# Performance work log

Measured on AMD Instinct MI355X. Metric: run time of the kernel, lower is better.

The kernel has to match this reference:

```python
import jax, jax.numpy as jnp
import numpy as np

SR = 16000
N_WT = 10
WT_LEN = 512
FIR_TAPS = 31
NU_C = 0.1
N_REFLECT = (FIR_TAPS - 1) // 2
B, L = 16, 160000


def setup_inputs() -> dict:
    key = jax.random.key(0)
    k1, k2, k3, k4 = jax.random.split(key, 4)
    # F0 in a realistic [100, 400) Hz range
    pitch = jax.random.uniform(k1, (B, L, 1), jnp.float32) * 300.0 + 100.0
    envelope = jax.random.uniform(k2, (B, L, 1), jnp.float32)
    # attention weights are 'already softmaxed' over the wavetable axis
    attention = jax.nn.softmax(jax.random.normal(k3, (B, L, N_WT), jnp.float32), axis=-1)
    # learned wavetables, init N(0, 0.01) as in the torch module (n_pure_harmonics=0)
    wavetables = jax.random.normal(k4, (N_WT, WT_LEN), jnp.float32) * 0.01
    # fixed windowed-sinc low-pass FIR (Type I), same construction as __init__
    n = np.arange(-(FIR_TAPS - 1) // 2, 1 + (FIR_TAPS - 1) // 2, dtype=np.float32)
    h = 2.0 * NU_C * np.sinc(2.0 * NU_C * n) * np.hamming(FIR_TAPS)
    fir_h = jnp.asarray(h, jnp.float32)
    return {"pitch": pitch, "envelope": envelope, "attention": attention,
            "wavetables": wavetables, "fir_h": fir_h}


def reference(pitch, envelope, attention, wavetables, fir_h):
    # circular ('reflect' in the repo's naming) pad each wavetable: (W, 512+2*15)
    wt_pad = jnp.concatenate(
        [wavetables[:, -N_REFLECT:], wavetables, wavetables[:, :N_REFLECT]], axis=1)
    # torch conv1d is cross-correlation; jnp.correlate 'valid' matches -> (W, 512)
    wt = jax.vmap(lambda x: jnp.correlate(x, fir_h, mode='valid'))(wt_pad)

    L_wt = WT_LEN
    freqs = pitch[..., 0]                       # (B, L)
    increment = (L_wt / SR) * freqs             # phase increment per sample
    # NOTE: faithful to torch code: increment[0] is the FIRST BATCH ROW (L,)
    index = jnp.cumsum(increment, axis=1) - increment[0]
    index = jnp.remainder(index, L_wt)
    index = jnp.where(L_wt - index < 1e-5, 0.0, index)
    idx_lo_f = jnp.floor(index)
    alpha = index - idx_lo_f                    # (B, L)
    i_lo = idx_lo_f.astype(jnp.int32)
    i_hi = jnp.ceil(index).astype(jnp.int32) % L_wt

    # gather all wavetables at once: (W, B, L)
    lo = jnp.take(wt, i_lo, axis=1)
    hi = jnp.take(wt, i_hi, axis=1)
    wave = lo + alpha[None, :, :] * (hi - lo)   # linear interpolation
    wave = jnp.transpose(wave, (1, 2, 0))       # (B, L, W)

    out = jnp.sum(wave * attention, axis=2, keepdims=True) * envelope  # (B, L, 1)
    return out
```

## Files before the change

kernel.cpp:

```cpp
#include <hip/hip_runtime.h>

#define N_WT_     10
#define WT_LEN_   512
#define FIR_TAPS_ 31
#define N_REFL_   15
#define B_        16
#define L_        160000

constexpr int   TPB   = 256;
constexpr float INCF  = 0.032f;
constexpr int   NG0   = L_ / 16;
constexpr int   NG1   = NG0 / 16;
constexpr int   NG2   = 40;
constexpr int   NG3   = 3;
constexpr int   CPB   = 5;

__global__ void fir_kernel(const float* __restrict__ wavetables,
                           const float* __restrict__ fir_h,
                           float* __restrict__ wt_out) {
    __shared__ float s_pad[WT_LEN_ + 2 * N_REFL_];
    __shared__ float s_h[FIR_TAPS_];
    const int w = blockIdx.x;
    const int i = threadIdx.x;
    if (i < FIR_TAPS_) s_h[i] = fir_h[i];
    for (int j = i; j < WT_LEN_ + 2 * N_REFL_; j += blockDim.x) {
        int src = (j + WT_LEN_ - N_REFL_) % WT_LEN_;
        s_pad[j] = wavetables[w * WT_LEN_ + src];
    }
    __syncthreads();
    float acc = 0.0f;
#pragma unroll
    for (int t = 0; t < FIR_TAPS_; ++t)
        acc = fmaf(s_h[t], s_pad[i + t], acc);
    wt_out[w * WT_LEN_ + i] = acc;
}

__global__ __launch_bounds__(TPB) void ysum_kernel(
        const float* __restrict__ pitch, float* __restrict__ y) {
    __shared__ float s_x[4096];
    const int b = blockIdx.y, bx = blockIdx.x, t = threadIdx.x;
    const float* prow = pitch + (size_t)b * L_;
    const int x0 = bx * 4096;
    for (int i = t; i < 4096; i += TPB) {
        int l = x0 + i;
        s_x[i] = (l < L_) ? INCF * prow[l] : 0.0f;
    }
    __syncthreads();
    const int g = bx * 256 + t;
    if (g < NG0) {
        const float* p = s_x + (g * 16 - x0);
        float acc = 0.0f;
        for (int i = 0; i < 16; ++i) acc += p[i];
        y[b * NG0 + g] = acc;
    }
}

__global__ __launch_bounds__(TPB) void scan_kernel(
        const float* __restrict__ y, float* __restrict__ S1) {
    __shared__ float s_y[NG0];
    __shared__ float s_S1[NG0];
    __shared__ float s_z[NG1];
    __shared__ float s_S2[NG1];
    __shared__ float s_w[NG2], s_S3[NG2];
    __shared__ float s_v[NG3], s_S4[NG3];
    const int b = blockIdx.x, t = threadIdx.x;
    const float* yrow = y + (size_t)b * NG0;
    for (int i = t; i < NG0; i += TPB) s_y[i] = yrow[i];
    __syncthreads();
    for (int j = t; j < NG1; j += TPB) {
        float a = 0.0f;
        for (int i = 0; i < 16; ++i) a += s_y[16 * j + i];
        s_z[j] = a;
    }
    __syncthreads();
    if (t < NG2) {
        float a = 0.0f;
        int hi = min(16 * t + 16, NG1);
        for (int i = 16 * t; i < hi; ++i) a += s_z[i];
        s_w[t] = a;
    }
    __syncthreads();
    if (t < NG3) {
        float a = 0.0f;
        int hi = min(16 * t + 16, NG2);
        for (int i = 16 * t; i < hi; ++i) a += s_w[i];
        s_v[t] = a;
    }
    __syncthreads();
    if (t == 0) {
        float run = 0.0f;
        for (int m = 0; m < NG3; ++m) { run += s_v[m]; s_S4[m] = run; }
    }
    __syncthreads();
    if (t < NG2) {
        float a = 0.0f;
        for (int i = (t >> 4) << 4; i <= t; ++i) a += s_w[i];
        if (t >= 16) a = a + s_S4[(t >> 4) - 1];
        s_S3[t] = a;
    }
    __syncthreads();
    if (t < NG2) {
        float r = 0.0f;
        float carry = (t > 0) ? s_S3[t - 1] : 0.0f;
        int hi = min(16 * t + 16, NG1);
        for (int k = 16 * t; k < hi; ++k) {
            r += s_z[k];
            s_S2[k] = (t > 0) ? r + carry : r;
        }
    }
    __syncthreads();
    for (int j = t; j < NG1; j += TPB) {
        float r = 0.0f;
        float carry = (j > 0) ? s_S2[j - 1] : 0.0f;
        for (int k = 0; k < 16; ++k) {
            r += s_y[16 * j + k];
            s_S1[16 * j + k] = (j > 0) ? r + carry : r;
        }
    }
    __syncthreads();
    float* S1row = S1 + (size_t)b * NG0;
    for (int i = t; i < NG0; i += TPB) S1row[i] = s_S1[i];
}

__global__ __launch_bounds__(TPB) void synth_kernel(
        const float* __restrict__ pitch,
        const float* __restrict__ envelope,
        const float* __restrict__ attention,
        const float* __restrict__ wt,
        const float* __restrict__ S1,
        float* __restrict__ out) {
    __shared__ float s_wt[N_WT_ * WT_LEN_];
    __shared__ float s_att[TPB * N_WT_];
    __shared__ float s_x[TPB];
    const int b = blockIdx.y, cb = blockIdx.x, t = threadIdx.x;

    const float4* wt4   = (const float4*)wt;
    float4*       s_wt4 = (float4*)s_wt;
    for (int i = t; i < N_WT_ * WT_LEN_ / 4; i += TPB) s_wt4[i] = wt4[i];

    const size_t rowb = (size_t)b * L_;

    for (int cc = 0; cc < CPB; ++cc) {
        const int    l0 = (cb * CPB + cc) * TPB;
        const int    l  = l0 + t;
        const size_t g  = rowb + l;
        __syncthreads();

        const float4* att4   = (const float4*)(attention + (rowb + l0) * N_WT_);
        float4*       s_att4 = (float4*)s_att;
        for (int i = t; i < TPB * N_WT_ / 4; i += TPB) s_att4[i] = att4[i];
        s_x[t] = INCF * pitch[g];
        __syncthreads();

        float acc = 0.0f;
        for (int i = t & ~15; i <= t; ++i) acc += s_x[i];
        const int g0 = l >> 4;
        if (g0 > 0) acc = acc + S1[(size_t)b * NG0 + (g0 - 1)];

        float idx = acc - INCF * pitch[l];
        float r = fmodf(idx, 512.0f);
        if (r < 0.0f) r += 512.0f;
        if (512.0f - r < 1e-5f) r = 0.0f;
        float fl = floorf(r);
        float alpha = r - fl;
        int lo = (int)fl;
        int hi = (int)ceilf(r);
        if (hi >= WT_LEN_) hi -= WT_LEN_;

        const float* a = s_att + t * N_WT_;
        float a0 = 0.0f;
#pragma unroll
        for (int w = 0; w < N_WT_; ++w) {
            float loV = s_wt[w * WT_LEN_ + lo];
            float hiV = s_wt[w * WT_LEN_ + hi];
            a0 += a[w] * (loV + alpha * (hiV - loV));
        }
        out[g] = a0 * envelope[g];
    }
}

extern "C" void kernel_launch(void* const* d_in, const int* in_sizes, int n_in,
                              void* d_out, int out_size, void* d_ws, size_t ws_size,
                              hipStream_t stream) {
    const float* pitch      = (const float*)d_in[0];
    const float* envelope   = (const float*)d_in[1];
    const float* attention  = (const float*)d_in[2];
    const float* wavetables = (const float*)d_in[3];
    const float* fir_h      = (const float*)d_in[4];
    float*       out        = (float*)d_out;

    char*  ws = (char*)d_ws;
    float* wt = (float*)(ws);
    float* y  = (float*)(ws + 32768);
    float* S1 = (float*)(ws + 32768 + 655360);

    fir_kernel<<<dim3(N_WT_), dim3(WT_LEN_), 0, stream>>>(wavetables, fir_h, wt);
    ysum_kernel<<<dim3(40, B_), dim3(TPB), 0, stream>>>(pitch, y);
    scan_kernel<<<dim3(B_), dim3(TPB), 0, stream>>>(y, S1);
    synth_kernel<<<dim3(L_ / (TPB * CPB), B_), dim3(TPB), 0, stream>>>(
        pitch, envelope, attention, wt, S1, out);
}
```

Before: 218.0 us.

## Interleave wavetables per index and drop shared staging in synth kernel

The FIR kernel now writes wavetables transposed as [index][table] with an extra wrap row, so one contiguous float2 read fetches all lo/hi samples. The synth kernel replaces the shared-memory pitch partial sum with wave shuffles and reads attention directly from global memory, removing the per-chunk block barriers and most shared memory. This aims to cut LDS bank conflicts, barrier stalls and occupancy limits, at the cost of uncoalesced-looking per-thread float2 attention loads.

```diff
diff --git a/kernel.cpp b/kernel.cpp
--- a/kernel.cpp
+++ b/kernel.cpp
@@ -14,10 +14,11 @@
 constexpr int   NG2   = 40;
 constexpr int   NG3   = 3;
 constexpr int   CPB   = 5;
+constexpr int   WTI   = (WT_LEN_ + 1) * N_WT_;
 
 __global__ void fir_kernel(const float* __restrict__ wavetables,
                            const float* __restrict__ fir_h,
-                           float* __restrict__ wt_out) {
+                           float* __restrict__ wt2) {
     __shared__ float s_pad[WT_LEN_ + 2 * N_REFL_];
     __shared__ float s_h[FIR_TAPS_];
     const int w = blockIdx.x;
@@ -32,7 +33,8 @@
 #pragma unroll
     for (int t = 0; t < FIR_TAPS_; ++t)
         acc = fmaf(s_h[t], s_pad[i + t], acc);
-    wt_out[w * WT_LEN_ + i] = acc;
+    wt2[i * N_WT_ + w] = acc;
+    if (i == 0) wt2[WT_LEN_ * N_WT_ + w] = acc;
 }
 
 __global__ __launch_bounds__(TPB) void ysum_kernel(
@@ -126,36 +128,33 @@
         const float* __restrict__ pitch,
         const float* __restrict__ envelope,
         const float* __restrict__ attention,
-        const float* __restrict__ wt,
+        const float* __restrict__ wt2,
         const float* __restrict__ S1,
         float* __restrict__ out) {
-    __shared__ float s_wt[N_WT_ * WT_LEN_];
-    __shared__ float s_att[TPB * N_WT_];
-    __shared__ float s_x[TPB];
+    __shared__ float s_wt[WTI];
     const int b = blockIdx.y, cb = blockIdx.x, t = threadIdx.x;
-
-    const float4* wt4   = (const float4*)wt;
-    float4*       s_wt4 = (float4*)s_wt;
-    for (int i = t; i < N_WT_ * WT_LEN_ / 4; i += TPB) s_wt4[i] = wt4[i];
-
+    for (int i = t; i < WTI; i += TPB) s_wt[i] = wt2[i];
+    __syncthreads();
+
+    const int lane = t & 63;
+    const int r16  = lane & 15;
+    const int sbase = lane & ~15;
     const size_t rowb = (size_t)b * L_;
+    const float* S1row = S1 + (size_t)b * NG0;
 
     for (int cc = 0; cc < CPB; ++cc) {
-        const int    l0 = (cb * CPB + cc) * TPB;
-        const int    l  = l0 + t;
-        const size_t g  = rowb + l;
-        __syncthreads();
-
-        const float4* att4   = (const float4*)(attention + (rowb + l0) * N_WT_);
-        float4*       s_att4 = (float4*)s_att;
-        for (int i = t; i < TPB * N_WT_ / 4; i += TPB) s_att4[i] = att4[i];
-        s_x[t] = INCF * pitch[g];
-        __syncthreads();
-
+        const int    l = (cb * CPB + cc) * TPB + t;
+        const size_t g = rowb + l;
+
+        float x = INCF * pitch[g];
         float acc = 0.0f;
-        for (int i = t & ~15; i <= t; ++i) acc += s_x[i];
+#pragma unroll
+        for (int k = 0; k < 16; ++k) {
+            float v = __shfl(x, sbase + k, 64);
+            acc += (k <= r16) ? v : 0.0f;
+        }
         const int g0 = l >> 4;
-        if (g0 > 0) acc = acc + S1[(size_t)b * NG0 + (g0 - 1)];
+        if (g0 > 0) acc = acc + S1row[g0 - 1];
 
         float idx = acc - INCF * pitch[l];
         float r = fmodf(idx, 512.0f);
@@ -164,17 +163,22 @@
         float fl = floorf(r);
         float alpha = r - fl;
         int lo = (int)fl;
-        int hi = (int)ceilf(r);
-        if (hi >= WT_LEN_) hi -= WT_LEN_;
-
-        const float* a = s_att + t * N_WT_;
+
+        const float2* pw = (const float2*)(s_wt + lo * N_WT_);
+        float2 q0 = pw[0], q1 = pw[1], q2 = pw[2], q3 = pw[3], q4 = pw[4];
+        float2 q5 = pw[5], q6 = pw[6], q7 = pw[7], q8 = pw[8], q9 = pw[9];
+        float loV[10] = {q0.x, q0.y, q1.x, q1.y, q2.x, q2.y, q3.x, q3.y, q4.x, q4.y};
+        float hiV[10] = {q5.x, q5.y, q6.x, q6.y, q7.x, q7.y, q8.x, q8.y, q9.x, q9.y};
+
+        const float2* ap = (const float2*)(attention + g * N_WT_);
+        float2 a01 = ap[0], a23 = ap[1], a45 = ap[2], a67 = ap[3], a89 = ap[4];
+        float a[10] = {a01.x, a01.y, a23.x, a23.y, a45.x, a45.y,
+                       a67.x, a67.y, a89.x, a89.y};
+
         float a0 = 0.0f;
 #pragma unroll
-        for (int w = 0; w < N_WT_; ++w) {
-            float loV = s_wt[w * WT_LEN_ + lo];
-            float hiV = s_wt[w * WT_LEN_ + hi];
-            a0 += a[w] * (loV + alpha * (hiV - loV));
-        }
+        for (int w = 0; w < N_WT_; ++w)
+            a0 += a[w] * (loV[w] + alpha * (hiV[w] - loV[w]));
         out[g] = a0 * envelope[g];
     }
 }
@@ -189,14 +193,14 @@
     const float* fir_h      = (const float*)d_in[4];
     float*       out        = (float*)d_out;
 
-    char*  ws = (char*)d_ws;
-    float* wt = (float*)(ws);
-    float* y  = (float*)(ws + 32768);
-    float* S1 = (float*)(ws + 32768 + 655360);
-
-    fir_kernel<<<dim3(N_WT_), dim3(WT_LEN_), 0, stream>>>(wavetables, fir_h, wt);
+    char*  ws  = (char*)d_ws;
+    float* wt2 = (float*)(ws);
+    float* y   = (float*)(ws + 32768);
+    float* S1  = (float*)(ws + 32768 + 655360);
+
+    fir_kernel<<<dim3(N_WT_), dim3(WT_LEN_), 0, stream>>>(wavetables, fir_h, wt2);
     ysum_kernel<<<dim3(40, B_), dim3(TPB), 0, stream>>>(pitch, y);
     scan_kernel<<<dim3(B_), dim3(TPB), 0, stream>>>(y, S1);
     synth_kernel<<<dim3(L_ / (TPB * CPB), B_), dim3(TPB), 0, stream>>>(
-        pitch, envelope, attention, wt, S1, out);
-}
+        pitch, envelope, attention, wt2, S1, out);
+}
```

After: 204.6 us. -6.1%, faster.
